# Performance work log

Measured on AMD Instinct MI355X. Metric: run time of the kernel, lower is better.

The kernel has to match this reference:

```python
import jax, jax.numpy as jnp
import numpy as np


def setup_inputs() -> dict:
    key = jax.random.key(0)
    k1, k2, k3, k4 = jax.random.split(key, 4)
    N, M, D = 4096, 4096, 1024
    H = jax.random.normal(k1, (N, D), dtype=jnp.float32)
    K = jax.random.normal(k2, (M, D), dtype=jnp.float32)
    V = jax.random.normal(k3, (M, D), dtype=jnp.float32)
    attn_mask = jax.random.uniform(k4, (N, M), dtype=jnp.float32)
    return {"H": H, "K": K, "V": V, "attn_mask": attn_mask}


def reference(H, K, V, attn_mask):
    # scores: [N, M] = H @ K^T, scaled by sqrt(d)
    d = H.shape[1]
    scores = jnp.matmul(H, K.T) / jnp.sqrt(jnp.asarray(d, dtype=H.dtype))
    # double softmax with elementwise mask multiply in between
    probs = jax.nn.softmax(jax.nn.softmax(scores, axis=1) * attn_mask, axis=1)
    return jnp.matmul(probs, V)
```

## Files before the change

### kernel.cpp

```cpp
#include <hip/hip_runtime.h>
#include <cstdint>

typedef unsigned short u16;
typedef __bf16 bf16x8 __attribute__((ext_vector_type(8)));
typedef float f32x4 __attribute__((ext_vector_type(4)));

__device__ __forceinline__ float bf2f(u16 h) {
  union { unsigned int u; float f; } v; v.u = ((unsigned int)h) << 16; return v.f;
}
__device__ __forceinline__ u16 f2bf(float f) {
  union { float f; unsigned int u; } v; v.f = f;
  unsigned int u = v.u;
  return (u16)((u + 0x7FFFu + ((u >> 16) & 1u)) >> 16);
}

__device__ __forceinline__ void ld_lds16(const void* g, void* l) {
  __builtin_amdgcn_global_load_lds(
      (const __attribute__((address_space(1))) unsigned int*)g,
      (__attribute__((address_space(3))) unsigned int*)l, 16, 0, 0);
}

template <int MODE>
__global__ __launch_bounds__(256, 2) void gemm_kernel(
    const u16* __restrict__ A, const u16* __restrict__ B,
    void* __restrict__ Cout, float* __restrict__ L1,
    const float* __restrict__ L2, int Kd, int Ncols)
{
  __shared__ u16 As[128 * 64];
  __shared__ u16 Bs[128 * 64];

  const int tid  = threadIdx.x;
  const int lane = tid & 63;
  const int w    = tid >> 6;
  const int wr   = w >> 1;
  const int wc   = w & 1;
  const int quad = lane >> 4;
  const int cIn  = lane & 15;

  const int rowBlk = blockIdx.y * 128;
  const int colBlk = blockIdx.x * 128;

  const int lrow   = lane >> 3;
  const int gchunk = (lane & 7) ^ lrow;

  f32x4 acc[4][4];
  #pragma unroll
  for (int i = 0; i < 4; ++i)
    #pragma unroll
    for (int j = 0; j < 4; ++j) acc[i][j] = {0.f, 0.f, 0.f, 0.f};

  for (int k0 = 0; k0 < Kd; k0 += 64) {
    #pragma unroll
    for (int t = 0; t < 4; ++t) {
      int rg = w * 4 + t;
      const u16* ga = A + (size_t)(rowBlk + rg * 8 + lrow) * Kd + k0 + gchunk * 8;
      const u16* gb = B + (size_t)(colBlk + rg * 8 + lrow) * Kd + k0 + gchunk * 8;
      ld_lds16(ga, &As[rg * 512]);
      ld_lds16(gb, &Bs[rg * 512]);
    }
    __syncthreads();

    #pragma unroll
    for (int ks = 0; ks < 2; ++ks) {
      bf16x8 af[4], bf[4];
      #pragma unroll
      for (int mi = 0; mi < 4; ++mi) {
        int row = wr * 64 + mi * 16 + cIn;
        int ch  = (ks * 4 + quad) ^ (row & 7);
        af[mi]  = *(const bf16x8*)&As[row * 64 + ch * 8];
      }
      #pragma unroll
      for (int ni = 0; ni < 4; ++ni) {
        int row = wc * 64 + ni * 16 + cIn;
        int ch  = (ks * 4 + quad) ^ (row & 7);
        bf[ni]  = *(const bf16x8*)&Bs[row * 64 + ch * 8];
      }
      #pragma unroll
      for (int mi = 0; mi < 4; ++mi)
        #pragma unroll
        for (int ni = 0; ni < 4; ++ni)
          acc[mi][ni] = __builtin_amdgcn_mfma_f32_16x16x32_bf16(
              af[mi], bf[ni], acc[mi][ni], 0, 0, 0);
    }
    __syncthreads();
  }

  if (MODE == 0) {
    u16* S = (u16*)Cout;
    const float scale = 0.03125f;
    #pragma unroll
    for (int mi = 0; mi < 4; ++mi) {
      float rs[4] = {0.f, 0.f, 0.f, 0.f};
      #pragma unroll
      for (int ni = 0; ni < 4; ++ni) {
        int col = colBlk + wc * 64 + ni * 16 + cIn;
        #pragma unroll
        for (int r = 0; r < 4; ++r) {
          int row = rowBlk + wr * 64 + mi * 16 + quad * 4 + r;
          u16 sb = f2bf(acc[mi][ni][r] * scale);
          S[(size_t)row * Ncols + col] = sb;
          rs[r] += __expf(bf2f(sb));
        }
      }
      #pragma unroll
      for (int m = 1; m < 16; m <<= 1)
        #pragma unroll
        for (int r = 0; r < 4; ++r) rs[r] += __shfl_xor(rs[r], m, 64);
      if (cIn == 0) {
        #pragma unroll
        for (int r = 0; r < 4; ++r)
          atomicAdd(&L1[rowBlk + wr * 64 + mi * 16 + quad * 4 + r], rs[r]);
      }
    }
  } else {
    float* Out = (float*)Cout;
    #pragma unroll
    for (int mi = 0; mi < 4; ++mi) {
      #pragma unroll
      for (int r = 0; r < 4; ++r) {
        int row   = rowBlk + wr * 64 + mi * 16 + quad * 4 + r;
        float inv = 1.0f / L2[row];
        #pragma unroll
        for (int ni = 0; ni < 4; ++ni) {
          int col = colBlk + wc * 64 + ni * 16 + cIn;
          Out[(size_t)row * Ncols + col] = acc[mi][ni][r] * inv;
        }
      }
    }
  }
}

__global__ void cvt_f32_bf16(const float* __restrict__ in, u16* __restrict__ out, int n4) {
  int i = blockIdx.x * blockDim.x + threadIdx.x;
  if (i < n4) {
    float4 v = ((const float4*)in)[i];
    ushort4 o;
    o.x = f2bf(v.x); o.y = f2bf(v.y); o.z = f2bf(v.z); o.w = f2bf(v.w);
    ((ushort4*)out)[i] = o;
  }
}

__global__ void transpose_cvt(const float* __restrict__ V, u16* __restrict__ Vt, int R, int C) {
  __shared__ float tile[32][33];
  int c0 = blockIdx.x * 32, r0 = blockIdx.y * 32;
  int tx = threadIdx.x, ty = threadIdx.y;
  #pragma unroll
  for (int i = 0; i < 32; i += 8)
    tile[ty + i][tx] = V[(size_t)(r0 + ty + i) * C + c0 + tx];
  __syncthreads();
  #pragma unroll
  for (int i = 0; i < 32; i += 8)
    Vt[(size_t)(c0 + ty + i) * R + r0 + tx] = f2bf(tile[tx][ty + i]);
}

__global__ __launch_bounds__(256) void softmax2_kernel(
    u16* __restrict__ S, const float* __restrict__ mask,
    const float* __restrict__ L1, float* __restrict__ L2, int M)
{
  int row = blockIdx.x;
  float inv = 1.0f / L1[row];
  u16* srow = S + (size_t)row * M;
  const float* mrow = mask + (size_t)row * M;
  float lsum = 0.f;
  for (int base = threadIdx.x * 16; base < M; base += blockDim.x * 16) {
    u16 sl[16];
    *(uint4*)(sl)     = *(const uint4*)(srow + base);
    *(uint4*)(sl + 8) = *(const uint4*)(srow + base + 8);
    float mv[16];
    #pragma unroll
    for (int q = 0; q < 4; ++q)
      *(float4*)(mv + q * 4) = *(const float4*)(mrow + base + q * 4);
    #pragma unroll
    for (int j = 0; j < 16; ++j) {
      float t = __expf(bf2f(sl[j])) * inv * mv[j];
      float p = __expf(t);
      lsum += p;
      sl[j] = f2bf(p);
    }
    *(uint4*)(srow + base)     = *(uint4*)(sl);
    *(uint4*)(srow + base + 8) = *(uint4*)(sl + 8);
  }
  #pragma unroll
  for (int m = 1; m < 64; m <<= 1) lsum += __shfl_xor(lsum, m, 64);
  __shared__ float wred[4];
  if ((threadIdx.x & 63) == 0) wred[threadIdx.x >> 6] = lsum;
  __syncthreads();
  if (threadIdx.x == 0) L2[row] = wred[0] + wred[1] + wred[2] + wred[3];
}

extern "C" void kernel_launch(void* const* d_in, const int* in_sizes, int n_in,
                              void* d_out, int out_size, void* d_ws, size_t ws_size,
                              hipStream_t stream) {
  const float* H    = (const float*)d_in[0];
  const float* Kin  = (const float*)d_in[1];
  const float* V    = (const float*)d_in[2];
  const float* mask = (const float*)d_in[3];
  float* out = (float*)d_out;

  const int N = 4096, M = 4096, D = 1024;

  char* ws = (char*)d_ws;
  u16*   Hb = (u16*)(ws);
  u16*   Kb = (u16*)(ws + (8ull << 20));
  u16*   Vt = (u16*)(ws + (16ull << 20));
  u16*   S  = (u16*)(ws + (24ull << 20));
  float* L1 = (float*)(ws + (56ull << 20));
  float* L2 = (float*)(ws + (56ull << 20) + 16384);

  hipMemsetAsync(L1, 0, 32768, stream);

  int n4 = N * D / 4;
  cvt_f32_bf16<<<dim3((n4 + 255) / 256), dim3(256), 0, stream>>>(H, Hb, n4);
  cvt_f32_bf16<<<dim3((n4 + 255) / 256), dim3(256), 0, stream>>>(Kin, Kb, n4);
  transpose_cvt<<<dim3(D / 32, M / 32), dim3(32, 8), 0, stream>>>(V, Vt, M, D);

  gemm_kernel<0><<<dim3(M / 128, N / 128), dim3(256), 0, stream>>>(
      Hb, Kb, S, L1, nullptr, D, M);
  softmax2_kernel<<<dim3(N), dim3(256), 0, stream>>>(S, mask, L1, L2, M);
  gemm_kernel<1><<<dim3(D / 128, N / 128), dim3(256), 0, stream>>>(
      S, Vt, out, nullptr, L2, M, D);
}
```

Before: 264.4 us.

## Split-K second GEMM with atomics, XCD-aware tile mapping, fuse prep kernels

The second GEMM (N=4096, D=1024) had only 256 tiles. It now splits K into 4 chunks, giving 1024 blocks that combine their results with float atomicAdd into an output zeroed by memset. Both GEMMs use a flat grid whose block-to-tile mapping groups tiles by XCD (blockIdx & 7) so each XCD's L2 sees more shared operand rows and columns. The three conversion/transpose kernels are merged into one launch to cut launch overhead. In exchange it adds an output memset and atomic traffic, and the summation order is no longer deterministic.

New measurement: 260.3 us. Within noise of the previous version (-1.6%).

```diff
diff --git a/kernel.cpp b/kernel.cpp
--- a/kernel.cpp
+++ b/kernel.cpp
@@ -24,7 +24,7 @@
 __global__ __launch_bounds__(256, 2) void gemm_kernel(
     const u16* __restrict__ A, const u16* __restrict__ B,
     void* __restrict__ Cout, float* __restrict__ L1,
-    const float* __restrict__ L2, int Kd, int Ncols)
+    const float* __restrict__ L2, int ldA, int ldB, int ldC)
 {
   __shared__ u16 As[128 * 64];
   __shared__ u16 Bs[128 * 64];
@@ -37,24 +37,35 @@
   const int quad = lane >> 4;
   const int cIn  = lane & 15;
 
-  const int rowBlk = blockIdx.y * 128;
-  const int colBlk = blockIdx.x * 128;
+  const int flat = blockIdx.x;
+  const int xcd  = flat & 7;
+  const int i    = flat >> 3;
+  int rowBlk, colBlk, kb, ke;
+  if (MODE == 0) {
+    rowBlk = ((xcd >> 2) * 16 + (i & 15)) * 128;
+    colBlk = ((xcd & 3) * 8 + (i >> 4)) * 128;
+    kb = 0; ke = 1024;
+  } else {
+    rowBlk = (((xcd & 1) * 16) + (i & 15)) * 128;
+    colBlk = (i >> 4) * 128;
+    kb = (xcd >> 1) * 1024; ke = kb + 1024;
+  }
 
   const int lrow   = lane >> 3;
   const int gchunk = (lane & 7) ^ lrow;
 
   f32x4 acc[4][4];
   #pragma unroll
-  for (int i = 0; i < 4; ++i)
-    #pragma unroll
-    for (int j = 0; j < 4; ++j) acc[i][j] = {0.f, 0.f, 0.f, 0.f};
-
-  for (int k0 = 0; k0 < Kd; k0 += 64) {
+  for (int a = 0; a < 4; ++a)
+    #pragma unroll
+    for (int b = 0; b < 4; ++b) acc[a][b] = {0.f, 0.f, 0.f, 0.f};
+
+  for (int k0 = kb; k0 < ke; k0 += 64) {
     #pragma unroll
     for (int t = 0; t < 4; ++t) {
       int rg = w * 4 + t;
-      const u16* ga = A + (size_t)(rowBlk + rg * 8 + lrow) * Kd + k0 + gchunk * 8;
-      const u16* gb = B + (size_t)(colBlk + rg * 8 + lrow) * Kd + k0 + gchunk * 8;
+      const u16* ga = A + (size_t)(rowBlk + rg * 8 + lrow) * ldA + k0 + gchunk * 8;
+      const u16* gb = B + (size_t)(colBlk + rg * 8 + lrow) * ldB + k0 + gchunk * 8;
       ld_lds16(ga, &As[rg * 512]);
       ld_lds16(gb, &Bs[rg * 512]);
     }
@@ -62,7 +73,7 @@
 
     #pragma unroll
     for (int ks = 0; ks < 2; ++ks) {
-      bf16x8 af[4], bf[4];
+      bf16x8 af[4], bfr[4];
       #pragma unroll
       for (int mi = 0; mi < 4; ++mi) {
         int row = wr * 64 + mi * 16 + cIn;
@@ -73,14 +84,14 @@
       for (int ni = 0; ni < 4; ++ni) {
         int row = wc * 64 + ni * 16 + cIn;
         int ch  = (ks * 4 + quad) ^ (row & 7);
-        bf[ni]  = *(const bf16x8*)&Bs[row * 64 + ch * 8];
+        bfr[ni] = *(const bf16x8*)&Bs[row * 64 + ch * 8];
       }
       #pragma unroll
       for (int mi = 0; mi < 4; ++mi)
         #pragma unroll
         for (int ni = 0; ni < 4; ++ni)
           acc[mi][ni] = __builtin_amdgcn_mfma_f32_16x16x32_bf16(
-              af[mi], bf[ni], acc[mi][ni], 0, 0, 0);
+              af[mi], bfr[ni], acc[mi][ni], 0, 0, 0);
     }
     __syncthreads();
   }
@@ -98,7 +109,7 @@
         for (int r = 0; r < 4; ++r) {
           int row = rowBlk + wr * 64 + mi * 16 + quad * 4 + r;
           u16 sb = f2bf(acc[mi][ni][r] * scale);
-          S[(size_t)row * Ncols + col] = sb;
+          S[(size_t)row * ldC + col] = sb;
           rs[r] += __expf(bf2f(sb));
         }
       }
@@ -123,34 +134,41 @@
         #pragma unroll
         for (int ni = 0; ni < 4; ++ni) {
           int col = colBlk + wc * 64 + ni * 16 + cIn;
-          Out[(size_t)row * Ncols + col] = acc[mi][ni][r] * inv;
+          atomicAdd(&Out[(size_t)row * ldC + col], acc[mi][ni][r] * inv);
         }
       }
     }
   }
 }
 
-__global__ void cvt_f32_bf16(const float* __restrict__ in, u16* __restrict__ out, int n4) {
-  int i = blockIdx.x * blockDim.x + threadIdx.x;
-  if (i < n4) {
-    float4 v = ((const float4*)in)[i];
+__global__ __launch_bounds__(256) void prep_kernel(
+    const float* __restrict__ H, const float* __restrict__ Kin,
+    const float* __restrict__ V, u16* __restrict__ Hb, u16* __restrict__ Kb,
+    u16* __restrict__ Vt)
+{
+  int b = blockIdx.x;
+  if (b < 8192) {
+    const float* src = (b < 4096) ? H : Kin;
+    u16* dst = (b < 4096) ? Hb : Kb;
+    int i = (b & 4095) * 256 + threadIdx.x;
+    float4 v = ((const float4*)src)[i];
     ushort4 o;
     o.x = f2bf(v.x); o.y = f2bf(v.y); o.z = f2bf(v.z); o.w = f2bf(v.w);
-    ((ushort4*)out)[i] = o;
-  }
-}
-
-__global__ void transpose_cvt(const float* __restrict__ V, u16* __restrict__ Vt, int R, int C) {
-  __shared__ float tile[32][33];
-  int c0 = blockIdx.x * 32, r0 = blockIdx.y * 32;
-  int tx = threadIdx.x, ty = threadIdx.y;
-  #pragma unroll
-  for (int i = 0; i < 32; i += 8)
-    tile[ty + i][tx] = V[(size_t)(r0 + ty + i) * C + c0 + tx];
-  __syncthreads();
-  #pragma unroll
-  for (int i = 0; i < 32; i += 8)
-    Vt[(size_t)(c0 + ty + i) * R + r0 + tx] = f2bf(tile[tx][ty + i]);
+    ((ushort4*)dst)[i] = o;
+  } else {
+    __shared__ float tile[32][33];
+    b -= 8192;
+    int c0 = (b & 31) * 32;
+    int r0 = (b >> 5) * 32;
+    int tx = threadIdx.x & 31, ty = threadIdx.x >> 5;
+    #pragma unroll
+    for (int s = 0; s < 32; s += 8)
+      tile[ty + s][tx] = V[(size_t)(r0 + ty + s) * 1024 + c0 + tx];
+    __syncthreads();
+    #pragma unroll
+    for (int s = 0; s < 32; s += 8)
+      Vt[(size_t)(c0 + ty + s) * 4096 + r0 + tx] = f2bf(tile[tx][ty + s]);
+  }
 }
 
 __global__ __launch_bounds__(256) void softmax2_kernel(
@@ -208,15 +226,13 @@
   float* L2 = (float*)(ws + (56ull << 20) + 16384);
 
   hipMemsetAsync(L1, 0, 32768, stream);
-
-  int n4 = N * D / 4;
-  cvt_f32_bf16<<<dim3((n4 + 255) / 256), dim3(256), 0, stream>>>(H, Hb, n4);
-  cvt_f32_bf16<<<dim3((n4 + 255) / 256), dim3(256), 0, stream>>>(Kin, Kb, n4);
-  transpose_cvt<<<dim3(D / 32, M / 32), dim3(32, 8), 0, stream>>>(V, Vt, M, D);
-
-  gemm_kernel<0><<<dim3(M / 128, N / 128), dim3(256), 0, stream>>>(
-      Hb, Kb, S, L1, nullptr, D, M);
+  hipMemsetAsync(out, 0, (size_t)N * D * sizeof(float), stream);
+
+  prep_kernel<<<dim3(12288), dim3(256), 0, stream>>>(H, Kin, V, Hb, Kb, Vt);
+
+  gemm_kernel<0><<<dim3(1024), dim3(256), 0, stream>>>(
+      Hb, Kb, S, L1, nullptr, D, D, M);
   softmax2_kernel<<<dim3(N), dim3(256), 0, stream>>>(S, mask, L1, L2, M);
-  gemm_kernel<1><<<dim3(D / 128, N / 128), dim3(256), 0, stream>>>(
-      S, Vt, out, nullptr, L2, M, D);
-}
+  gemm_kernel<1><<<dim3(1024), dim3(256), 0, stream>>>(
+      S, Vt, out, nullptr, L2, M, M, D);
+}
```
